# Kernel optimization log

Measured on AMD Instinct MI355X. Metric: run time of the kernel, lower is better.

Reference implementation:

```python
import jax, jax.numpy as jnp
import numpy as np

VOCAB, EMB, HID, OUT = 32000, 512, 1024, 512
B, S = 64, 256


def setup_inputs() -> dict:
    key = jax.random.key(0)
    ks = jax.random.split(key, 16)
    def xavier(k, shape):
        bound = np.sqrt(6.0 / (shape[0] + shape[1]))
        return jax.random.uniform(k, shape, jnp.float32, -bound, bound)
    return {
        "tokens": jax.random.randint(ks[0], (B, S), 0, VOCAB),
        "emb": jax.random.normal(ks[1], (VOCAB, EMB), jnp.float32) * 0.02,
        "W_xi": xavier(ks[2], (EMB, HID)),
        "W_xf": xavier(ks[3], (EMB, HID)),
        "W_xo": xavier(ks[4], (EMB, HID)),
        "W_xc": xavier(ks[5], (EMB, HID)),
        "W_hi": xavier(ks[6], (HID, HID)),
        "W_hf": xavier(ks[7], (HID, HID)),
        "W_ho": xavier(ks[8], (HID, HID)),
        "W_hc": xavier(ks[9], (HID, HID)),
        "W_hy": xavier(ks[10], (HID, OUT)),
        "b_i": jnp.zeros((HID,), jnp.float32),
        "b_f": jnp.zeros((HID,), jnp.float32),
        "b_o": jnp.zeros((HID,), jnp.float32),
        "b_c": jnp.zeros((HID,), jnp.float32),
        "b_hy": jnp.zeros((OUT,), jnp.float32),
    }


def reference(tokens, emb, W_xi, W_xf, W_xo, W_xc, W_hi, W_hf, W_ho, W_hc,
              W_hy, b_i, b_f, b_o, b_c, b_hy):
    # Embedding lookup for all timesteps (dropout is identity at inference).
    x = emb[tokens]  # [B, S, E]
    # Precompute input-to-gate projections in one batched GEMM per gate.
    gx_i = jnp.einsum('bse,eh->bsh', x, W_xi) + b_i
    gx_f = jnp.einsum('bse,eh->bsh', x, W_xf) + b_f
    gx_o = jnp.einsum('bse,eh->bsh', x, W_xo) + b_o
    gx_c = jnp.einsum('bse,eh->bsh', x, W_xc) + b_c
    # Time-major stacked gates: [S, B, 4, H]
    g = jnp.stack([gx_i, gx_f, gx_o, gx_c], axis=2).transpose(1, 0, 2, 3)

    h0 = jnp.zeros((tokens.shape[0], W_hi.shape[0]), x.dtype)
    c0 = jnp.zeros_like(h0)

    def step(carry, g_t):
        h, c = carry
        i = jax.nn.sigmoid(g_t[:, 0] + h @ W_hi)
        f = jax.nn.sigmoid(g_t[:, 1] + h @ W_hf)
        o = jax.nn.sigmoid(g_t[:, 2] + h @ W_ho)
        cc = jnp.tanh(g_t[:, 3] + h @ W_hc)
        c = f * c + i * cc
        h = o * jnp.tanh(c)
        return (h, c), None

    (h, c), _ = jax.lax.scan(step, (h0, c0), g)
    return h @ W_hy + b_hy  # [B, OUT]
```

## Files before the change

### kernel.cpp

```cpp
#include <hip/hip_runtime.h>
#include <hip/hip_bf16.h>

#define EMBN   512
#define HIDN   1024
#define OUTN   512
#define BBN    64
#define SSN    256
#define NBLK   256
#define PSTR   20

typedef __attribute__((ext_vector_type(8))) short bf16x8;
typedef __attribute__((ext_vector_type(4))) float f32x4;
typedef unsigned short us;
typedef unsigned long long ull;

static __device__ __forceinline__ us f2bf(float x) {
  unsigned int u = __float_as_uint(x);
  unsigned int r = (u + 0x7fffu + ((u >> 16) & 1u)) >> 16;
  return (us)r;
}
static __device__ __forceinline__ float bf2f(us u) {
  unsigned int v = ((unsigned int)u) << 16;
  return __uint_as_float(v);
}

__global__ void pack_w(const float* __restrict__ wxi, const float* __restrict__ wxf,
                       const float* __restrict__ wxo, const float* __restrict__ wxc,
                       const float* __restrict__ whi, const float* __restrict__ whf,
                       const float* __restrict__ who, const float* __restrict__ whc,
                       us* __restrict__ Whip, us* __restrict__ Wlop) {
  int idx = blockIdx.x * 256 + threadIdx.x;
  int lane = idx & 63;
  int kt   = (idx >> 6) % 48;
  int j    = idx / (48 * 64);
  int q = lane & 15, g = q >> 2, r = q & 3;
  int hd = 4 * j + r;
  int kb = kt * 32 + ((lane >> 4) << 3);
  const float* wx = (g == 0) ? wxi : (g == 1) ? wxf : (g == 2) ? wxo : wxc;
  const float* wh = (g == 0) ? whi : (g == 1) ? whf : (g == 2) ? who : whc;
  long obase = (long)idx * 8;
  #pragma unroll
  for (int jj = 0; jj < 8; ++jj) {
    int k = kb + jj;
    float v = (k < EMBN) ? wx[(long)k * HIDN + hd] : wh[(long)(k - EMBN) * HIDN + hd];
    us hi = f2bf(v);
    us lo = f2bf(v - bf2f(hi));
    Whip[obase + jj] = hi;
    Wlop[obase + jj] = lo;
  }
}

__global__ void pack_x(const int* __restrict__ tokens, const float* __restrict__ emb,
                       us* __restrict__ Xhi, us* __restrict__ Xlo) {
  int idx = blockIdx.x * 256 + threadIdx.x;
  int k = idx & 511;
  int b = (idx >> 9) & 63;
  int t = idx >> 15;
  int tok = tokens[b * SSN + t];
  float v = emb[(long)tok * EMBN + k];
  us hi = f2bf(v);
  Xhi[idx] = hi;
  Xlo[idx] = f2bf(v - bf2f(hi));
}

#define XISS(A, c) { _Pragma("unroll") for (int q = 0; q < 4; ++q) { \
      A[2*q]   = *(const bf16x8*)(xh + (((c)*4 + q) << 5)); \
      A[2*q+1] = *(const bf16x8*)(xl + (((c)*4 + q) << 5)); } }
#define XCON(A, c) { _Pragma("unroll") for (int q = 0; q < 4; ++q) { \
      const int kt = (c)*4 + q; \
      bf16x8 w0 = *(const bf16x8*)(WHi + (kt << 9) + (lane << 3)); \
      bf16x8 w1 = *(const bf16x8*)(WLo + (kt << 9) + (lane << 3)); \
      accA = __builtin_amdgcn_mfma_f32_16x16x32_bf16(w0, A[2*q],   accA, 0, 0, 0); \
      accB = __builtin_amdgcn_mfma_f32_16x16x32_bf16(w0, A[2*q+1], accB, 0, 0, 0); \
      accC = __builtin_amdgcn_mfma_f32_16x16x32_bf16(w1, A[2*q],   accC, 0, 0, 0); } }
#define HISS(A, c) { _Pragma("unroll") for (int q = 0; q < 4; ++q) { \
      A[2*q]   = *(const bf16x8*)(hh + (((c)*4 + q) << 5)); \
      A[2*q+1] = *(const bf16x8*)(hl + (((c)*4 + q) << 5)); } }
#define HCON(A, c) { _Pragma("unroll") for (int q = 0; q < 4; ++q) { \
      const int kt = 16 + (c)*4 + q; \
      bf16x8 w0 = *(const bf16x8*)(WHi + (kt << 9) + (lane << 3)); \
      bf16x8 w1 = *(const bf16x8*)(WLo + (kt << 9) + (lane << 3)); \
      accA = __builtin_amdgcn_mfma_f32_16x16x32_bf16(w0, A[2*q],   accA, 0, 0, 0); \
      accB = __builtin_amdgcn_mfma_f32_16x16x32_bf16(w0, A[2*q+1], accB, 0, 0, 0); \
      accC = __builtin_amdgcn_mfma_f32_16x16x32_bf16(w1, A[2*q],   accC, 0, 0, 0); } }

__launch_bounds__(256, 1)
__global__ void lstm_persist(const us* __restrict__ Whip, const us* __restrict__ Wlop,
                             const us* __restrict__ Xhi, const us* __restrict__ Xlo,
                             us* Hhi, us* Hlo, float* hfin, int* flags,
                             const float* __restrict__ biP, const float* __restrict__ bfP,
                             const float* __restrict__ boP, const float* __restrict__ bcP,
                             int useInv) {
  extern __shared__ char smem[];
  us* WHi = (us*)smem;
  us* WLo = WHi + 24576;
  float* preact = (float*)(smem + 98304);

  const int j = blockIdx.x, tid = threadIdx.x;
  const int wv = tid >> 6, lane = tid & 63;

  {
    const uint4* shi = (const uint4*)(Whip + (long)j * 24576);
    const uint4* slo = (const uint4*)(Wlop + (long)j * 24576);
    uint4* dhi = (uint4*)WHi;
    uint4* dlo = (uint4*)WLo;
    for (int i = tid; i < 3072; i += 256) { dhi[i] = shi[i]; dlo[i] = slo[i]; }
  }
  const int gb = tid >> 2, gr = tid & 3;
  const float bi_r = biP[4 * j + gr], bf_r = bfP[4 * j + gr];
  const float bo_r = boP[4 * j + gr], bc_r = bcP[4 * j + gr];
  float c_reg = 0.f;

  const int mrow = (wv << 4) + (lane & 15);
  const int kj = (lane >> 4) << 3;
  const int p0 = (lane >> 4) << 2;
  __syncthreads();

  #pragma unroll 1
  for (int t = 0; t < SSN; ++t) {
    f32x4 accA = {0.f, 0.f, 0.f, 0.f};
    f32x4 accB = {0.f, 0.f, 0.f, 0.f};
    f32x4 accC = {0.f, 0.f, 0.f, 0.f};

    {
      const us* xh = Xhi + ((long)t << 15) + (mrow << 9) + kj;
      const us* xl = Xlo + ((long)t << 15) + (mrow << 9) + kj;
      bf16x8 XA[8], XB[8];
      XISS(XA, 0) XISS(XB, 1)
      __builtin_amdgcn_sched_barrier(0);
      XCON(XA, 0) XISS(XA, 2)
      __builtin_amdgcn_sched_barrier(0);
      XCON(XB, 1) XISS(XB, 3)
      __builtin_amdgcn_sched_barrier(0);
      XCON(XA, 2) XCON(XB, 3)
    }

    if (t > 0) {
      while (__hip_atomic_load(&flags[tid], __ATOMIC_RELAXED, __HIP_MEMORY_SCOPE_AGENT) < t) {
        __builtin_amdgcn_s_sleep(1);
      }
      __syncthreads();
      if (useInv) __builtin_amdgcn_fence(__ATOMIC_ACQUIRE, "agent");

      const int cur = useInv ? (t % 3) : t;
      const us* hh = Hhi + (((long)cur * BBN + mrow) << 10) + kj;
      const us* hl = Hlo + (((long)cur * BBN + mrow) << 10) + kj;
      bf16x8 HA[8], HB[8], HC[8], HD[8];
      HISS(HA, 0) HISS(HB, 1) HISS(HC, 2) HISS(HD, 3)
      __builtin_amdgcn_sched_barrier(0);
      HCON(HA, 0) HISS(HA, 4)
      __builtin_amdgcn_sched_barrier(0);
      HCON(HB, 1) HISS(HB, 5)
      __builtin_amdgcn_sched_barrier(0);
      HCON(HC, 2) HISS(HC, 6)
      __builtin_amdgcn_sched_barrier(0);
      HCON(HD, 3) HISS(HD, 7)
      __builtin_amdgcn_sched_barrier(0);
      HCON(HA, 4) HCON(HB, 5) HCON(HC, 6) HCON(HD, 7)
    }

    {
      f32x4 acc = accA + accB;
      acc = acc + accC;
      *(f32x4*)(preact + mrow * PSTR + p0) = acc;
    }
    __syncthreads();

    {
      float pi = preact[gb * PSTR + gr]      + bi_r;
      float pf = preact[gb * PSTR + 4 + gr]  + bf_r;
      float po = preact[gb * PSTR + 8 + gr]  + bo_r;
      float pc = preact[gb * PSTR + 12 + gr] + bc_r;
      float vi = 1.f / (1.f + expf(-pi));
      float vf = 1.f / (1.f + expf(-pf));
      float vo = 1.f / (1.f + expf(-po));
      float vc = tanhf(pc);
      c_reg = vf * c_reg + vi * vc;
      float h = vo * tanhf(c_reg);
      if (t == SSN - 1) hfin[(gb << 10) + 4 * j + gr] = h;
      us hh_ = f2bf(h);
      us hl_ = f2bf(h - bf2f(hh_));

      unsigned int hpair = (unsigned int)hh_ | ((unsigned int)hl_ << 16);
      const int base = lane & ~3;
      unsigned int g0 = (unsigned int)__shfl((int)hpair, base);
      unsigned int g1 = (unsigned int)__shfl((int)hpair, base + 1);
      unsigned int g2 = (unsigned int)__shfl((int)hpair, base + 2);
      unsigned int g3 = (unsigned int)__shfl((int)hpair, base + 3);
      unsigned int hi01 = (g0 & 0xffffu) | (g1 << 16);
      unsigned int hi23 = (g2 & 0xffffu) | (g3 << 16);
      unsigned int lo01 = (g0 >> 16)     | (g1 & 0xffff0000u);
      unsigned int lo23 = (g2 >> 16)     | (g3 & 0xffff0000u);
      ull hiq = ((ull)hi23 << 32) | (ull)hi01;
      ull loq = ((ull)lo23 << 32) | (ull)lo01;

      if (!useInv) {
        const long nxt = t + 1;
        if (gr == 0) {
          __hip_atomic_store((ull*)(Hhi + ((nxt * BBN + gb) << 10) + 4 * j), hiq,
                             __ATOMIC_RELAXED, __HIP_MEMORY_SCOPE_AGENT);
          __hip_atomic_store((ull*)(Hlo + ((nxt * BBN + gb) << 10) + 4 * j), loq,
                             __ATOMIC_RELAXED, __HIP_MEMORY_SCOPE_AGENT);
        }
        asm volatile("s_waitcnt vmcnt(0)" ::: "memory");
        __syncthreads();
        if (tid == 0)
          __hip_atomic_store(&flags[j], t + 1, __ATOMIC_RELAXED, __HIP_MEMORY_SCOPE_AGENT);
      } else {
        const long nxt = (t + 1) % 3;
        if (gr == 0) {
          *(ull*)(Hhi + ((nxt * BBN + gb) << 10) + 4 * j) = hiq;
          *(ull*)(Hlo + ((nxt * BBN + gb) << 10) + 4 * j) = loq;
        }
        __syncthreads();
        if (tid == 0)
          __hip_atomic_store(&flags[j], t + 1, __ATOMIC_RELEASE, __HIP_MEMORY_SCOPE_AGENT);
      }
    }
  }
}

__global__ void out_gemm(const float* __restrict__ hfin, const float* __restrict__ Why,
                         const float* __restrict__ bhy, float* __restrict__ out) {
  int b = blockIdx.x, n = threadIdx.x;
  const float* h = hfin + (b << 10);
  float acc = 0.f;
  #pragma unroll 8
  for (int k = 0; k < HIDN; ++k) acc = fmaf(h[k], Why[(k << 9) + n], acc);
  out[(b << 9) + n] = acc + bhy[n];
}

extern "C" void kernel_launch(void* const* d_in, const int* in_sizes, int n_in,
                              void* d_out, int out_size, void* d_ws, size_t ws_size,
                              hipStream_t stream) {
  const int*   tokens = (const int*)d_in[0];
  const float* emb    = (const float*)d_in[1];
  const float* Wxi    = (const float*)d_in[2];
  const float* Wxf    = (const float*)d_in[3];
  const float* Wxo    = (const float*)d_in[4];
  const float* Wxc    = (const float*)d_in[5];
  const float* Whi_   = (const float*)d_in[6];
  const float* Whf    = (const float*)d_in[7];
  const float* Who    = (const float*)d_in[8];
  const float* Whc    = (const float*)d_in[9];
  const float* Why    = (const float*)d_in[10];
  const float* bi     = (const float*)d_in[11];
  const float* bfv    = (const float*)d_in[12];
  const float* bo     = (const float*)d_in[13];
  const float* bc     = (const float*)d_in[14];
  const float* bhy    = (const float*)d_in[15];
  float* outp = (float*)d_out;

  char* ws = (char*)d_ws;
  size_t off = 0;
  auto carve = [&](size_t bytes) -> void* {
    void* p = ws + off;
    off += (bytes + 255) & ~(size_t)255;
    return p;
  };
  us*    Whip = (us*)carve(12582912);
  us*    Wlop = (us*)carve(12582912);
  us*    Xhi  = (us*)carve(16777216);
  us*    Xlo  = (us*)carve(16777216);
  float* hfin = (float*)carve(262144);
  int*   flags = (int*)carve(1024);

  const size_t bigBytes = (size_t)(SSN + 1) * BBN * HIDN * 2;
  int useInv;
  us *Hhi, *Hlo;
  if (ws_size >= off + 2 * ((bigBytes + 255) & ~(size_t)255)) {
    useInv = 0;
    Hhi = (us*)carve(bigBytes);
    Hlo = (us*)carve(bigBytes);
  } else {
    useInv = 1;
    Hhi = (us*)carve((size_t)3 * BBN * HIDN * 2);
    Hlo = (us*)carve((size_t)3 * BBN * HIDN * 2);
  }

  if (ws_size < off) {
    (void)hipMemsetAsync(d_out, 0, (size_t)out_size * 4, stream);
    return;
  }

  (void)hipMemsetAsync(flags, 0, 1024, stream);

  pack_w<<<3072, 256, 0, stream>>>(Wxi, Wxf, Wxo, Wxc, Whi_, Whf, Who, Whc, Whip, Wlop);
  pack_x<<<32768, 256, 0, stream>>>(tokens, emb, Xhi, Xlo);

  (void)hipFuncSetAttribute((const void*)lstm_persist,
                            hipFuncAttributeMaxDynamicSharedMemorySize, 103424);
  lstm_persist<<<NBLK, 256, 103424, stream>>>(Whip, Wlop, Xhi, Xlo, Hhi, Hlo,
                                              hfin, flags, bi, bfv, bo, bc, useInv);
  out_gemm<<<BBN, OUTN, 0, stream>>>(hfin, Why, bhy, outp);
}
```

Baseline: 3.181 ms.

## Poll flags with one wave using vector loads and use power-of-two hidden-state ring

The per-step barrier now has only wave 0 poll all 256 block flags, each lane reading four at once with a dwordx4 load that bypasses the cache, and exits when no lane sees a stale flag. Before, every thread spun on its own flag with a sleep. The hidden-state buffer becomes a power-of-two ring sized to the workspace (up to 256 slots), replacing the old choice between a full buffer and a 3-slot buffer. An acquire fence is issued only when the ring wraps, which drops most per-step fences when the workspace is small. This trades fewer polling loads and fences for reliance on relaxed stores plus cache-bypass loads for cross-block visibility.

```diff
diff --git a/kernel.cpp b/kernel.cpp
--- a/kernel.cpp
+++ b/kernel.cpp
@@ -11,6 +11,7 @@
 
 typedef __attribute__((ext_vector_type(8))) short bf16x8;
 typedef __attribute__((ext_vector_type(4))) float f32x4;
+typedef __attribute__((ext_vector_type(4))) int int4v;
 typedef unsigned short us;
 typedef unsigned long long ull;
 
@@ -90,7 +91,7 @@
                              us* Hhi, us* Hlo, float* hfin, int* flags,
                              const float* __restrict__ biP, const float* __restrict__ bfP,
                              const float* __restrict__ boP, const float* __restrict__ bcP,
-                             int useInv) {
+                             int K) {
   extern __shared__ char smem[];
   us* WHi = (us*)smem;
   us* WLo = WHi + 24576;
@@ -98,6 +99,8 @@
 
   const int j = blockIdx.x, tid = threadIdx.x;
   const int wv = tid >> 6, lane = tid & 63;
+  const int Km = K - 1;
+  const bool ROT = (K != 256);
 
   {
     const uint4* shi = (const uint4*)(Whip + (long)j * 24576);
@@ -136,13 +139,20 @@
     }
 
     if (t > 0) {
-      while (__hip_atomic_load(&flags[tid], __ATOMIC_RELAXED, __HIP_MEMORY_SCOPE_AGENT) < t) {
-        __builtin_amdgcn_s_sleep(1);
+      if (wv == 0) {
+        const int* fp = flags + (lane << 2);
+        int4v f;
+        do {
+          asm volatile("global_load_dwordx4 %0, %1, off sc0 sc1\n\t"
+                       "s_waitcnt vmcnt(0)"
+                       : "=&v"(f) : "v"(fp) : "memory");
+        } while (__any((f.x < t) | (f.y < t) | (f.z < t) | (f.w < t)));
       }
       __syncthreads();
-      if (useInv) __builtin_amdgcn_fence(__ATOMIC_ACQUIRE, "agent");
-
-      const int cur = useInv ? (t % 3) : t;
+      if (ROT && (t & Km) == 0)
+        __builtin_amdgcn_fence(__ATOMIC_ACQUIRE, "agent");
+
+      const int cur = t & Km;
       const us* hh = Hhi + (((long)cur * BBN + mrow) << 10) + kj;
       const us* hl = Hlo + (((long)cur * BBN + mrow) << 10) + kj;
       bf16x8 HA[8], HB[8], HC[8], HD[8];
@@ -194,28 +204,17 @@
       ull hiq = ((ull)hi23 << 32) | (ull)hi01;
       ull loq = ((ull)lo23 << 32) | (ull)lo01;
 
-      if (!useInv) {
-        const long nxt = t + 1;
-        if (gr == 0) {
-          __hip_atomic_store((ull*)(Hhi + ((nxt * BBN + gb) << 10) + 4 * j), hiq,
-                             __ATOMIC_RELAXED, __HIP_MEMORY_SCOPE_AGENT);
-          __hip_atomic_store((ull*)(Hlo + ((nxt * BBN + gb) << 10) + 4 * j), loq,
-                             __ATOMIC_RELAXED, __HIP_MEMORY_SCOPE_AGENT);
-        }
-        asm volatile("s_waitcnt vmcnt(0)" ::: "memory");
-        __syncthreads();
-        if (tid == 0)
-          __hip_atomic_store(&flags[j], t + 1, __ATOMIC_RELAXED, __HIP_MEMORY_SCOPE_AGENT);
-      } else {
-        const long nxt = (t + 1) % 3;
-        if (gr == 0) {
-          *(ull*)(Hhi + ((nxt * BBN + gb) << 10) + 4 * j) = hiq;
-          *(ull*)(Hlo + ((nxt * BBN + gb) << 10) + 4 * j) = loq;
-        }
-        __syncthreads();
-        if (tid == 0)
-          __hip_atomic_store(&flags[j], t + 1, __ATOMIC_RELEASE, __HIP_MEMORY_SCOPE_AGENT);
+      const long nxt = (t + 1) & Km;
+      if (gr == 0) {
+        __hip_atomic_store((ull*)(Hhi + ((nxt * BBN + gb) << 10) + 4 * j), hiq,
+                           __ATOMIC_RELAXED, __HIP_MEMORY_SCOPE_AGENT);
+        __hip_atomic_store((ull*)(Hlo + ((nxt * BBN + gb) << 10) + 4 * j), loq,
+                           __ATOMIC_RELAXED, __HIP_MEMORY_SCOPE_AGENT);
       }
+      asm volatile("s_waitcnt vmcnt(0)" ::: "memory");
+      __syncthreads();
+      if (tid == 0)
+        __hip_atomic_store(&flags[j], t + 1, __ATOMIC_RELAXED, __HIP_MEMORY_SCOPE_AGENT);
     }
   }
 }
@@ -265,23 +264,15 @@
   float* hfin = (float*)carve(262144);
   int*   flags = (int*)carve(1024);
 
-  const size_t bigBytes = (size_t)(SSN + 1) * BBN * HIDN * 2;
-  int useInv;
-  us *Hhi, *Hlo;
-  if (ws_size >= off + 2 * ((bigBytes + 255) & ~(size_t)255)) {
-    useInv = 0;
-    Hhi = (us*)carve(bigBytes);
-    Hlo = (us*)carve(bigBytes);
-  } else {
-    useInv = 1;
-    Hhi = (us*)carve((size_t)3 * BBN * HIDN * 2);
-    Hlo = (us*)carve((size_t)3 * BBN * HIDN * 2);
-  }
-
-  if (ws_size < off) {
+  size_t rem = (ws_size > off) ? (ws_size - off) : 0;
+  int K = 256;
+  while (K > 4 && (size_t)2 * (size_t)K * 131072 + 512 > rem) K >>= 1;
+  if ((size_t)2 * (size_t)K * 131072 + 512 > rem) {
     (void)hipMemsetAsync(d_out, 0, (size_t)out_size * 4, stream);
     return;
   }
+  us* Hhi = (us*)carve((size_t)K * 131072);
+  us* Hlo = (us*)carve((size_t)K * 131072);
 
   (void)hipMemsetAsync(flags, 0, 1024, stream);
 
@@ -291,6 +282,6 @@
   (void)hipFuncSetAttribute((const void*)lstm_persist,
                             hipFuncAttributeMaxDynamicSharedMemorySize, 103424);
   lstm_persist<<<NBLK, 256, 103424, stream>>>(Whip, Wlop, Xhi, Xlo, Hhi, Hlo,
-                                              hfin, flags, bi, bfv, bo, bc, useInv);
+                                              hfin, flags, bi, bfv, bo, bc, K);
   out_gemm<<<BBN, OUTN, 0, stream>>>(hfin, Why, bhy, outp);
 }
```

Measured after the change: 3.150 ms. Within noise of the previous version (-1.0%).
